# Performance work log

Measured on AMD Instinct MI355X. Metric: run time of the kernel, lower is better.

Reference implementation:

```python
import jax, jax.numpy as jnp
import numpy as np

H = 1024
B_SZ = 4
L = 2048


def setup_inputs() -> dict:
    key = jax.random.key(0)
    ks = jax.random.split(key, 7)
    s_in = 1.0 / np.sqrt(H)
    x = jax.random.normal(ks[0], (B_SZ, L, H), dtype=jnp.float32)
    # torch nn.Linear weights: (out_features, in_features)
    W_proj = jax.random.uniform(ks[1], (4 * H, H), minval=-s_in, maxval=s_in, dtype=jnp.float32)
    W_delta = jax.random.uniform(ks[2], (H, H), minval=-s_in, maxval=s_in, dtype=jnp.float32)
    b_delta = jax.random.uniform(ks[3], (H,), minval=-s_in, maxval=s_in, dtype=jnp.float32)
    A = 0.02 * jax.random.normal(ks[4], (1, 1, H), dtype=jnp.float32)
    Bp = 0.02 * jax.random.normal(ks[5], (1, H, 1), dtype=jnp.float32)
    D = jnp.ones((1,), dtype=jnp.float32)
    return {"x": x, "W_proj": W_proj, "A": A, "Bp": Bp, "D": D, "W_delta": W_delta, "b_delta": b_delta}


def reference(x, W_proj, A, Bp, D, W_delta, b_delta):
    # x: (b, l, h)
    h = x.shape[-1]
    proj = x @ W_proj.T                                   # (b, l, 4h)
    delta, Bs, Cs, residual = jnp.split(proj, 4, axis=-1) # each (b, l, h)
    delta = jax.nn.softplus(delta @ W_delta.T + b_delta)  # (b, l, h)
    A1 = A[0, 0]       # (h,)
    B1 = Bp[0, :, 0]   # (h,)
    # discretization: dA[b,h,l] = exp(delta*A)[b,l,h] * B1[h] (n-dim of Bp has size 1)
    dA = jnp.exp(delta * A1) * B1                         # (b, l, h), layout transposed vs torch
    # dB[b,h,0,l] = cumsum_l(delta[b,l,h] * B1[h])
    dB = jnp.cumsum(delta * B1, axis=1)                   # (b, l, h)
    # selective_scan: y[b,h,l] = sum_n (dA[b,h,l]*u[b,h,n] + dB[b,h,0,l]) * C[b,h,n]
    # sum over n distributes: y = dA * sum_n(u*C) + dB * sum_n(C)
    uC = jnp.sum(x * Cs, axis=1, keepdims=True)           # (b, 1, h)
    Csum = jnp.sum(Cs, axis=1, keepdims=True)             # (b, 1, h)
    y = dA * uC + dB * Csum                               # (b, l, h)
    return y + residual * D
```

## Files before the change

kernel.cpp:

```cpp
#include <hip/hip_runtime.h>
#include <hip/hip_bf16.h>
#include <cstdint>

#define H 1024
#define BSZ 4
#define LSEQ 2048
#define M_TOT (BSZ*LSEQ)
#define NCH 32
#define LCH (LSEQ/NCH)

typedef __attribute__((ext_vector_type(4))) float  f32x4;
typedef __attribute__((ext_vector_type(2))) float  f32x2;
typedef __attribute__((ext_vector_type(8))) __bf16 bf16x8;
typedef __attribute__((ext_vector_type(4))) __bf16 bf16x4;
typedef __attribute__((ext_vector_type(2))) __bf16 bf16x2;

typedef __attribute__((address_space(1))) unsigned int as1_u32;
typedef __attribute__((address_space(3))) unsigned int as3_u32;

__device__ __forceinline__ void gld_lds16(const void* g, const void* l) {
    as1_u32* gp = reinterpret_cast<as1_u32*>((uintptr_t)g);
    as3_u32* lp = reinterpret_cast<as3_u32*>((uint32_t)(uintptr_t)l);
    __builtin_amdgcn_global_load_lds(gp, lp, 16, 0, 0);
}

__device__ __forceinline__ float softplus_fast(float f) {
    return fmaxf(f, 0.f) + __logf(1.f + __expf(-fabsf(f)));
}

template<int KT, int MODE>
__global__ __launch_bounds__(256, 3) void gemm_bt(
    const __bf16* __restrict__ A,
    const __bf16* __restrict__ B,
    __bf16* __restrict__ O0,
    __bf16* __restrict__ O2,
    const __bf16* __restrict__ xb,
    const float* __restrict__ bias,
    float* __restrict__ pD,
    float* __restrict__ pUp,
    float* __restrict__ pCp)
{
    constexpr int K = KT * 32;
    __shared__ __align__(16) __bf16 lds[17408];

    const int tid  = threadIdx.x;
    const int lane = tid & 63;
    const int wid  = tid >> 6;
    const int wr   = (wid >> 1) * 64;
    const int wc   = (wid & 1) * 64;
    const int l15  = lane & 15;
    const int quad = lane >> 4;

    const int row0 = blockIdx.y * 128;
    const int col0 = blockIdx.x * 128;

    const int srow = lane >> 2;
    const int soct = (lane & 3) ^ ((lane >> 3) & 3);
    const __bf16* ag0 = A + (size_t)(row0 + (wid    )*16 + srow) * K + soct*8;
    const __bf16* ag1 = A + (size_t)(row0 + (wid + 4)*16 + srow) * K + soct*8;
    const __bf16* bg0 = B + (size_t)(col0 + (wid    )*16 + srow) * K + soct*8;
    const __bf16* bg1 = B + (size_t)(col0 + (wid + 4)*16 + srow) * K + soct*8;
    const int lA0 = (wid    )*512;
    const int lA1 = (wid + 4)*512;
    const int lB0 = 4096 + (wid    )*512;
    const int lB1 = 4096 + (wid + 4)*512;

    const int sw = (l15 >> 1) & 3;
    int aoff[4], boff[4];
#pragma unroll
    for (int i = 0; i < 4; ++i) {
        aoff[i] =        ((wr + i*16 + l15) * 4 + (quad ^ sw)) * 8;
        boff[i] = 4096 + ((wc + i*16 + l15) * 4 + (quad ^ sw)) * 8;
    }

    f32x4 acc[4][4] = {};

    auto stage = [&](int buf) {
        __bf16* base = lds + buf * 8192;
        gld_lds16(ag0, base + lA0);
        gld_lds16(ag1, base + lA1);
        gld_lds16(bg0, base + lB0);
        gld_lds16(bg1, base + lB1);
        ag0 += 32; ag1 += 32; bg0 += 32; bg1 += 32;
    };
    auto compute = [&](int buf) {
        const __bf16* base = lds + buf * 8192;
        bf16x8 af[4], bf[4];
#pragma unroll
        for (int i = 0; i < 4; ++i) af[i] = *(const bf16x8*)(base + aoff[i]);
#pragma unroll
        for (int j = 0; j < 4; ++j) bf[j] = *(const bf16x8*)(base + boff[j]);
#pragma unroll
        for (int i = 0; i < 4; ++i)
#pragma unroll
            for (int j = 0; j < 4; ++j)
                acc[i][j] = __builtin_amdgcn_mfma_f32_16x16x32_bf16(
                    af[i], bf[j], acc[i][j], 0, 0, 0);
    };

    stage(0);
#pragma unroll 2
    for (int kt = 0; kt < KT; ++kt) {
        __syncthreads();
        if (kt + 1 < KT) stage((kt + 1) & 1);
        compute(kt & 1);
    }

    const int colb = (col0 & 1023) + wc + l15;
    const int rowb = row0 + wr + quad*4;

    if (MODE == 0) {
#pragma unroll
        for (int i = 0; i < 4; ++i)
#pragma unroll
            for (int j = 0; j < 4; ++j) {
                const int col = colb + j*16;
#pragma unroll
                for (int r = 0; r < 4; ++r)
                    O0[(size_t)(rowb + i*16 + r) * H + col] = (__bf16)acc[i][j][r];
            }
    } else {
        const int seg = col0 >> 10;
        if (seg == 0) {
            const int chunk = (row0 + wr) >> 6;
#pragma unroll
            for (int j = 0; j < 4; ++j) {
                const int col = colb + j*16;
                const float bv = bias[col];
                float s = 0.f;
#pragma unroll
                for (int i = 0; i < 4; ++i)
#pragma unroll
                    for (int r = 0; r < 4; ++r) {
                        float f = softplus_fast(acc[i][j][r] + bv);
                        O0[(size_t)(rowb + i*16 + r) * H + col] = (__bf16)f;
                        s += f;
                    }
                s += __shfl_down(s, 32); s += __shfl_down(s, 16);
                if (quad == 0) pD[chunk*H + col] = s;
            }
        } else if (seg == 1) {
            __syncthreads();
#pragma unroll
            for (int i = 0; i < 4; ++i)
#pragma unroll
                for (int j = 0; j < 4; ++j) {
                    const int lrow0 = wr + quad*4 + i*16;
                    const int lcol  = wc + j*16 + l15;
#pragma unroll
                    for (int r = 0; r < 4; ++r)
                        lds[(lrow0 + r)*136 + lcol] = (__bf16)acc[i][j][r];
                }
            __syncthreads();
            const int g   = tid >> 4;
            const int oct = tid & 15;
            const int gc0 = (col0 & 1023) + oct*8;
            float su[8] = {}, sc[8] = {};
#pragma unroll
            for (int rr = 0; rr < 8; ++rr) {
                const int lrow = g*8 + rr;
                bf16x8 cv = *(const bf16x8*)(lds + lrow*136 + oct*8);
                bf16x8 xv = *(const bf16x8*)(xb + (size_t)(row0 + lrow)*H + gc0);
#pragma unroll
                for (int q = 0; q < 8; ++q) {
                    float c = (float)cv[q];
                    su[q] += (float)xv[q] * c;
                    sc[q] += c;
                }
            }
            float* pf = reinterpret_cast<float*>(lds);
            __syncthreads();
#pragma unroll
            for (int q = 0; q < 8; ++q) {
                pf[g*128 + oct*8 + q]        = su[q];
                pf[2048 + g*128 + oct*8 + q] = sc[q];
            }
            __syncthreads();
            const int col = tid & 127;
            const int rb  = row0 >> 7;
            float s = 0.f;
            if (tid < 128) {
#pragma unroll
                for (int g2 = 0; g2 < 16; ++g2) s += pf[g2*128 + col];
                pUp[rb*H + (col0 & 1023) + col] = s;
            } else {
#pragma unroll
                for (int g2 = 0; g2 < 16; ++g2) s += pf[2048 + g2*128 + col];
                pCp[rb*H + (col0 & 1023) + col] = s;
            }
        } else {
#pragma unroll
            for (int i = 0; i < 4; ++i)
#pragma unroll
                for (int j = 0; j < 4; ++j) {
                    const int col = colb + j*16;
#pragma unroll
                    for (int r = 0; r < 4; ++r)
                        O2[(size_t)(rowb + i*16 + r) * H + col] = (__bf16)acc[i][j][r];
                }
        }
    }
}

#define XB 8192
#define PB 2048
#define DB 1024
#define TB 256
__global__ void cast_kernel(const float* __restrict__ x,
                            const float* __restrict__ Wp,
                            const float* __restrict__ Wd,
                            __bf16* __restrict__ xb,
                            __bf16* __restrict__ Wpb,
                            __bf16* __restrict__ Wdb,
                            __bf16* __restrict__ Wp1T)
{
    __shared__ __bf16 tlds[64*65];
    const int t = threadIdx.x;
    const int bidx = blockIdx.x;

    if (bidx < XB + PB + DB) {
        const f32x4* src; __bf16* dst; int si, di;
        if (bidx < XB) {
            int i = bidx*256 + t;
            src = (const f32x4*)x;  si = i; dst = xb;  di = i;
        } else if (bidx < XB + PB) {
            int j = (bidx - XB)*256 + t;
            int row = j >> 8, cf = j & 255;
            src = (const f32x4*)Wp; si = (2048 + row)*256 + cf;
            dst = Wpb; di = (1024 + row)*256 + cf;
        } else {
            int j = (bidx - XB - PB)*256 + t;
            src = (const f32x4*)Wd; si = j; dst = Wdb; di = j;
        }
        f32x4 v = src[si];
        bf16x4 o = { (__bf16)v[0], (__bf16)v[1], (__bf16)v[2], (__bf16)v[3] };
        *(bf16x4*)(dst + (size_t)di*4) = o;
    } else {
        int tt = bidx - (XB + PB + DB);
        int ty = tt >> 4, tx = tt & 15;
        int rb = t >> 4, cb = t & 15;
#pragma unroll
        for (int rr = 0; rr < 4; ++rr) {
            int row = rb*4 + rr;
            f32x4 v = *(const f32x4*)(Wp + (size_t)(ty*64 + row)*1024 + tx*64 + cb*4);
#pragma unroll
            for (int q = 0; q < 4; ++q)
                tlds[row*65 + cb*4 + q] = (__bf16)v[q];
        }
        __syncthreads();
#pragma unroll
        for (int rr = 0; rr < 4; ++rr) {
            int kk = rb*4 + rr;
            bf16x4 o = { tlds[(cb*4+0)*65 + kk], tlds[(cb*4+1)*65 + kk],
                         tlds[(cb*4+2)*65 + kk], tlds[(cb*4+3)*65 + kk] };
            *(bf16x4*)(Wp1T + (size_t)(tx*64 + kk)*1024 + ty*64 + cb*4) = o;
        }
    }
}

__global__ void final_kernel(const __bf16* __restrict__ delta,
                             const __bf16* __restrict__ res,
                             const float* __restrict__ pD,
                             const float* __restrict__ pUp,
                             const float* __restrict__ pCp,
                             const float* __restrict__ Av,
                             const float* __restrict__ Bv,
                             const float* __restrict__ Dv,
                             float* __restrict__ out)
{
    const int c = blockIdx.x, b = blockIdx.z;
    const int h0 = blockIdx.y * 512 + threadIdx.x * 2;
    float run0 = 0.f, run1 = 0.f;
    for (int cp = 0; cp < c; ++cp) {
        f32x2 v = *(const f32x2*)(pD + (b*NCH + cp)*H + h0);
        run0 += v[0]; run1 += v[1];
    }
    float uc0 = 0.f, uc1 = 0.f, cs0 = 0.f, cs1 = 0.f;
#pragma unroll
    for (int i = 0; i < 16; ++i) {
        f32x2 u = *(const f32x2*)(pUp + (b*16 + i)*H + h0);
        f32x2 s = *(const f32x2*)(pCp + (b*16 + i)*H + h0);
        uc0 += u[0]; uc1 += u[1]; cs0 += s[0]; cs1 += s[1];
    }
    const f32x2 a1 = *(const f32x2*)(Av + h0);
    const f32x2 b1 = *(const f32x2*)(Bv + h0);
    const float dd = Dv[0];
    size_t base = ((size_t)(b*LSEQ + c*LCH)) * H + h0;
    for (int l = 0; l < LCH; ++l) {
        size_t idx = base + (size_t)l * H;
        bf16x2 dv2 = *(const bf16x2*)(delta + idx);
        bf16x2 rs2 = *(const bf16x2*)(res + idx);
        float d0 = (float)dv2[0], d1v = (float)dv2[1];
        run0 += d0; run1 += d1v;
        f32x2 o;
        o[0] = __expf(d0*a1[0])*b1[0]*uc0 + run0*b1[0]*cs0 + (float)rs2[0]*dd;
        o[1] = __expf(d1v*a1[1])*b1[1]*uc1 + run1*b1[1]*cs1 + (float)rs2[1]*dd;
        *(f32x2*)(out + idx) = o;
    }
}

extern "C" void kernel_launch(void* const* d_in, const int* in_sizes, int n_in,
                              void* d_out, int out_size, void* d_ws, size_t ws_size,
                              hipStream_t stream)
{
    (void)in_sizes; (void)n_in; (void)out_size; (void)ws_size;
    const float* x  = (const float*)d_in[0];
    const float* Wp = (const float*)d_in[1];
    const float* Av = (const float*)d_in[2];
    const float* Bv = (const float*)d_in[3];
    const float* Dv = (const float*)d_in[4];
    const float* Wd = (const float*)d_in[5];
    const float* bd = (const float*)d_in[6];
    float* out = (float*)d_out;

    char* ws = (char*)d_ws;
    size_t o = 0;
    auto alloc = [&](size_t bytes) {
        void* p = ws + o; o += (bytes + 255) & ~(size_t)255; return p;
    };
    __bf16* xb   = (__bf16*)alloc((size_t)M_TOT * H * 2);
    __bf16* Wpb  = (__bf16*)alloc((size_t)3072 * H * 2);
    __bf16* Wdb  = (__bf16*)alloc((size_t)H * H * 2);
    __bf16* Wp1T = (__bf16*)alloc((size_t)H * H * 2);
    __bf16* resb = (__bf16*)alloc((size_t)M_TOT * H * 2);
    __bf16* db   = (__bf16*)alloc((size_t)M_TOT * H * 2);
    float*  pD   = (float*)alloc((size_t)BSZ * NCH * H * 4);
    float*  pUp  = (float*)alloc((size_t)64 * H * 4);
    float*  pCp  = (float*)alloc((size_t)64 * H * 4);

    cast_kernel<<<XB + PB + DB + TB, 256, 0, stream>>>(
        x, Wp, Wd, xb, Wpb, Wdb, Wp1T);
    gemm_bt<32, 0><<<dim3(8, 8), 256, 0, stream>>>(
        Wdb, Wp1T, Wpb, nullptr, nullptr, nullptr, nullptr, nullptr, nullptr);
    gemm_bt<32, 2><<<dim3(24, 64), 256, 0, stream>>>(
        xb, Wpb, db, resb, xb, bd, pD, pUp, pCp);
    final_kernel<<<dim3(NCH, 2, BSZ), 256, 0, stream>>>(db, resb, pD, pUp, pCp,
                                                        Av, Bv, Dv, out);
}
```

Before: 206.0 us.

## Replace main projection GEMM with 256x256-tile, 8-wave software-pipelined kernel

The large x@W_proj GEMM moves from a 128x128-tile kernel with 4 waves to a new 256x256-tile kernel with 8 waves and 128 KB of double-buffered LDS. Loads go straight to LDS through an XOR swizzle and are interleaved with MFMA phases using explicit barriers, vmcnt waits and setprio. The fused epilogues (softplus with chunk sums, the uC/Csum reductions, the residual store) are rewritten for the larger tile, and a swizzled grid order is added for L2 locality. This is meant to increase data reuse and overlap memory with compute, but it raises register and LDS pressure, and only 384 blocks may leave the device underfilled.

```diff
diff --git a/kernel.cpp b/kernel.cpp
--- a/kernel.cpp
+++ b/kernel.cpp
@@ -119,85 +119,225 @@
                 for (int r = 0; r < 4; ++r)
                     O0[(size_t)(rowb + i*16 + r) * H + col] = (__bf16)acc[i][j][r];
             }
-    } else {
-        const int seg = col0 >> 10;
-        if (seg == 0) {
-            const int chunk = (row0 + wr) >> 6;
-#pragma unroll
-            for (int j = 0; j < 4; ++j) {
-                const int col = colb + j*16;
-                const float bv = bias[col];
+    }
+    (void)xb; (void)bias; (void)pD; (void)pUp; (void)pCp; (void)O2;
+}
+
+
+#define BAR()    asm volatile("s_barrier" ::: "memory")
+#define WAITV2() asm volatile("s_waitcnt vmcnt(2)" ::: "memory")
+
+#define STAGE_A(d, h, kt) do {                                               \
+    const __bf16* g_ = Asrc + (size_t)((h)*128) * H + (kt)*64;               \
+    const __bf16* l_ = lds + (d)*32768 + ((h)*128)*64 + lwave;               \
+    gld_lds16(g_,          l_);                                              \
+    gld_lds16(g_ + 64*H,   l_ + 64*64);                                      \
+} while(0)
+
+#define STAGE_B(d, h, kt) do {                                               \
+    const __bf16* g_ = Bsrc + (size_t)((h)*128) * H + (kt)*64;               \
+    const __bf16* l_ = lds + (d)*32768 + 16384 + ((h)*128)*64 + lwave;       \
+    gld_lds16(g_,          l_);                                              \
+    gld_lds16(g_ + 64*H,   l_ + 64*64);                                      \
+} while(0)
+
+#define RD_A(d, mh) do {                                                     \
+    const __bf16* base_ = lds + (d)*32768;                                   \
+    _Pragma("unroll")                                                        \
+    for (int ii = 0; ii < 4; ++ii) {                                         \
+        af[ii][0] = *(const bf16x8*)(base_ + aoff[(mh)*4 + ii]);             \
+        af[ii][1] = *(const bf16x8*)(base_ + (aoff[(mh)*4 + ii] ^ 32));      \
+    }                                                                        \
+} while(0)
+
+#define RD_B(d, nh) do {                                                     \
+    const __bf16* base_ = lds + (d)*32768;                                   \
+    _Pragma("unroll")                                                        \
+    for (int jj = 0; jj < 2; ++jj) {                                         \
+        bf[(nh)*2+jj][0] = *(const bf16x8*)(base_ + boff[(nh)*2 + jj]);      \
+        bf[(nh)*2+jj][1] = *(const bf16x8*)(base_ + (boff[(nh)*2 + jj] ^ 32)); \
+    }                                                                        \
+} while(0)
+
+#define MM(mh, nh) do {                                                      \
+    __builtin_amdgcn_s_setprio(1);                                           \
+    _Pragma("unroll")                                                        \
+    for (int ii = 0; ii < 4; ++ii)                                           \
+    _Pragma("unroll")                                                        \
+    for (int jj = 0; jj < 2; ++jj)                                           \
+    _Pragma("unroll")                                                        \
+    for (int kk = 0; kk < 2; ++kk)                                           \
+        acc[(mh)*4+ii][(nh)*2+jj] = __builtin_amdgcn_mfma_f32_16x16x32_bf16( \
+            af[ii][kk], bf[(nh)*2+jj][kk], acc[(mh)*4+ii][(nh)*2+jj], 0,0,0);\
+    __builtin_amdgcn_s_setprio(0);                                           \
+} while(0)
+
+__global__ __launch_bounds__(512, 2) void gemm256(
+    const __bf16* __restrict__ A,
+    const __bf16* __restrict__ B,
+    __bf16* __restrict__ O0,
+    __bf16* __restrict__ O2,
+    const __bf16* __restrict__ xb,
+    const float* __restrict__ bias,
+    float* __restrict__ pD,
+    float* __restrict__ pUp,
+    float* __restrict__ pCp)
+{
+    __shared__ __align__(16) __bf16 lds[65536];
+
+    const int tid  = threadIdx.x;
+    const int lane = tid & 63;
+    const int wid  = tid >> 6;
+    const int l15  = lane & 15;
+    const int quad = lane >> 4;
+    const int wrv  = (wid >> 2) * 128;
+    const int wcv  = (wid & 3) * 64;
+
+    const int bid = blockIdx.x;
+    const int swz = (bid & 7) * 48 + (bid >> 3);
+    const int bx = swz % 12;
+    const int by = swz / 12;
+    const int row0 = by * 256;
+    const int col0 = bx * 256;
+
+    const int lg = (tid & 7) ^ ((tid >> 3) & 7);
+    const __bf16* Asrc = A + (size_t)(row0 + (tid >> 3)) * H + lg * 8;
+    const __bf16* Bsrc = B + (size_t)(col0 + (tid >> 3)) * H + lg * 8;
+    const int lwave = wid * 8 * 64;
+
+    int aoff[8], boff[4];
+#pragma unroll
+    for (int i = 0; i < 8; ++i)
+        aoff[i] = (wrv + i*16 + l15)*64 + ((quad ^ (l15 & 7)) << 3);
+#pragma unroll
+    for (int j = 0; j < 4; ++j)
+        boff[j] = 16384 + (wcv + j*16 + l15)*64 + ((quad ^ (l15 & 7)) << 3);
+
+    f32x4 acc[8][4] = {};
+    bf16x8 af[4][2], bf[4][2];
+
+    STAGE_A(0,0,0); STAGE_A(0,1,0); STAGE_B(0,0,0); STAGE_B(0,1,0);
+    STAGE_A(1,0,1);
+
+#pragma unroll 1
+    for (int it = 0; it < 8; ++it) {
+        const int t1 = 2*it + 1;
+        const int t2 = (it < 7) ? 2*it + 2 : 15;
+        const int t3 = (it < 7) ? 2*it + 3 : 15;
+        WAITV2(); BAR();
+        RD_A(0,0); RD_B(0,0);
+        STAGE_A(1,1,t1);
+        BAR(); MM(0,0); BAR();
+        RD_B(0,1);
+        STAGE_B(1,0,t1);
+        BAR(); MM(0,1); BAR();
+        RD_A(0,1);
+        STAGE_B(1,1,t1);
+        BAR(); MM(1,0); BAR();
+        STAGE_A(0,0,t2);
+        BAR(); MM(1,1); BAR();
+        WAITV2(); BAR();
+        RD_A(1,0); RD_B(1,0);
+        STAGE_A(0,1,t2);
+        BAR(); MM(0,0); BAR();
+        RD_B(1,1);
+        STAGE_B(0,0,t2);
+        BAR(); MM(0,1); BAR();
+        RD_A(1,1);
+        STAGE_B(0,1,t2);
+        BAR(); MM(1,0); BAR();
+        STAGE_A(1,0,t3);
+        BAR(); MM(1,1); BAR();
+    }
+    asm volatile("s_waitcnt vmcnt(0)" ::: "memory");
+    __syncthreads();
+
+    const int seg   = col0 >> 10;
+    const int cbase = col0 & 1023;
+    const int colb  = cbase + wcv + l15;
+    const int rowb  = row0 + wrv + quad*4;
+
+    if (seg == 0) {
+        const int chunkb = (row0 + wrv) >> 6;
+#pragma unroll
+        for (int j = 0; j < 4; ++j) {
+            const int col = colb + j*16;
+            const float bv = bias[col];
+#pragma unroll
+            for (int ih = 0; ih < 2; ++ih) {
                 float s = 0.f;
 #pragma unroll
-                for (int i = 0; i < 4; ++i)
+                for (int ii = 0; ii < 4; ++ii) {
+                    const int i = ih*4 + ii;
 #pragma unroll
                     for (int r = 0; r < 4; ++r) {
                         float f = softplus_fast(acc[i][j][r] + bv);
                         O0[(size_t)(rowb + i*16 + r) * H + col] = (__bf16)f;
                         s += f;
                     }
+                }
                 s += __shfl_down(s, 32); s += __shfl_down(s, 16);
-                if (quad == 0) pD[chunk*H + col] = s;
+                if (quad == 0) pD[(chunkb + ih)*H + col] = s;
             }
-        } else if (seg == 1) {
-            __syncthreads();
-#pragma unroll
-            for (int i = 0; i < 4; ++i)
-#pragma unroll
-                for (int j = 0; j < 4; ++j) {
-                    const int lrow0 = wr + quad*4 + i*16;
-                    const int lcol  = wc + j*16 + l15;
-#pragma unroll
-                    for (int r = 0; r < 4; ++r)
-                        lds[(lrow0 + r)*136 + lcol] = (__bf16)acc[i][j][r];
-                }
-            __syncthreads();
-            const int g   = tid >> 4;
-            const int oct = tid & 15;
-            const int gc0 = (col0 & 1023) + oct*8;
-            float su[8] = {}, sc[8] = {};
-#pragma unroll
-            for (int rr = 0; rr < 8; ++rr) {
-                const int lrow = g*8 + rr;
-                bf16x8 cv = *(const bf16x8*)(lds + lrow*136 + oct*8);
-                bf16x8 xv = *(const bf16x8*)(xb + (size_t)(row0 + lrow)*H + gc0);
-#pragma unroll
-                for (int q = 0; q < 8; ++q) {
-                    float c = (float)cv[q];
-                    su[q] += (float)xv[q] * c;
-                    sc[q] += c;
+        }
+    } else if (seg == 2) {
+#pragma unroll
+        for (int i = 0; i < 8; ++i)
+#pragma unroll
+            for (int j = 0; j < 4; ++j) {
+                const int col = colb + j*16;
+#pragma unroll
+                for (int r = 0; r < 4; ++r)
+                    O2[(size_t)(rowb + i*16 + r) * H + col] = (__bf16)acc[i][j][r];
+            }
+    } else {
+#pragma unroll
+        for (int i = 0; i < 8; ++i)
+#pragma unroll
+            for (int j = 0; j < 4; ++j) {
+                const int lcol = wcv + j*16 + l15;
+#pragma unroll
+                for (int r = 0; r < 4; ++r) {
+                    const int lrow = wrv + i*16 + quad*4 + r;
+                    lds[lrow*256 + (((lcol>>3) ^ ((lrow>>2)&7))<<3) + (lcol&7)]
+                        = (__bf16)acc[i][j][r];
                 }
             }
-            float* pf = reinterpret_cast<float*>(lds);
-            __syncthreads();
+        __syncthreads();
+        const int g = tid >> 5, oct = tid & 31;
+        const int gc0 = cbase + oct*8;
+        float su[8] = {}, sc[8] = {};
+#pragma unroll
+        for (int rr = 0; rr < 16; ++rr) {
+            const int lrow = g*16 + rr;
+            bf16x8 cv = *(const bf16x8*)(lds + lrow*256 +
+                                         ((oct ^ ((lrow>>2)&7)) << 3));
+            bf16x8 xv = *(const bf16x8*)(xb + (size_t)(row0 + lrow)*H + gc0);
 #pragma unroll
             for (int q = 0; q < 8; ++q) {
-                pf[g*128 + oct*8 + q]        = su[q];
-                pf[2048 + g*128 + oct*8 + q] = sc[q];
+                float c = (float)cv[q];
+                su[q] += (float)xv[q] * c;
+                sc[q] += c;
             }
-            __syncthreads();
-            const int col = tid & 127;
-            const int rb  = row0 >> 7;
+        }
+        float* pf = reinterpret_cast<float*>(lds);
+        __syncthreads();
+#pragma unroll
+        for (int q = 0; q < 8; ++q) {
+            pf[g*256 + oct*8 + q]        = su[q];
+            pf[4096 + g*256 + oct*8 + q] = sc[q];
+        }
+        __syncthreads();
+        const int col = tid & 255;
+        const int sel = tid >> 8;
+#pragma unroll
+        for (int rb2 = 0; rb2 < 2; ++rb2) {
             float s = 0.f;
-            if (tid < 128) {
-#pragma unroll
-                for (int g2 = 0; g2 < 16; ++g2) s += pf[g2*128 + col];
-                pUp[rb*H + (col0 & 1023) + col] = s;
-            } else {
-#pragma unroll
-                for (int g2 = 0; g2 < 16; ++g2) s += pf[2048 + g2*128 + col];
-                pCp[rb*H + (col0 & 1023) + col] = s;
-            }
-        } else {
-#pragma unroll
-            for (int i = 0; i < 4; ++i)
-#pragma unroll
-                for (int j = 0; j < 4; ++j) {
-                    const int col = colb + j*16;
-#pragma unroll
-                    for (int r = 0; r < 4; ++r)
-                        O2[(size_t)(rowb + i*16 + r) * H + col] = (__bf16)acc[i][j][r];
-                }
+#pragma unroll
+            for (int g2 = 0; g2 < 8; ++g2)
+                s += pf[sel*4096 + (rb2*8 + g2)*256 + col];
+            float* dst = sel ? pCp : pUp;
+            dst[(size_t)((row0 >> 7) + rb2)*H + cbase + col] = s;
         }
     }
 }
@@ -332,7 +472,7 @@
         x, Wp, Wd, xb, Wpb, Wdb, Wp1T);
     gemm_bt<32, 0><<<dim3(8, 8), 256, 0, stream>>>(
         Wdb, Wp1T, Wpb, nullptr, nullptr, nullptr, nullptr, nullptr, nullptr);
-    gemm_bt<32, 2><<<dim3(24, 64), 256, 0, stream>>>(
+    gemm256<<<dim3(384), 512, 0, stream>>>(
         xb, Wpb, db, resb, xb, bd, pD, pUp, pCp);
     final_kernel<<<dim3(NCH, 2, BSZ), 256, 0, stream>>>(db, resb, pD, pUp, pCp,
                                                         Av, Bv, Dv, out);
```

Result: no change. 202.4 us (-1.8%).

## Replace main projection GEMM with 256x128 triple-buffered pipelined kernel

Applied to the files above, without the earlier changes.

Adds a new 512-thread GEMM kernel with 256x128 tiles, K-step 64, triple-buffered direct global-to-LDS loads with explicit vmcnt waits, split half-K fragment loads, s_setprio around MFMAs, and a grouped block swizzle for L2 reuse. It replaces the 128x128 double-buffered kernel for the main x @ W projection, aiming to hide load latency and raise MFMA utilisation. The C-segment reduction is rewritten to use an XOR-swizzled LDS layout without padding. The final kernel is relaunched with smaller blocks and more of them. The larger LDS footprint (144KB) limits occupancy, and the hand-written waits have to match the order in which stages are issued.

```diff
diff --git a/kernel.cpp b/kernel.cpp
--- a/kernel.cpp
+++ b/kernel.cpp
@@ -32,16 +32,10 @@
 __global__ __launch_bounds__(256, 3) void gemm_bt(
     const __bf16* __restrict__ A,
     const __bf16* __restrict__ B,
-    __bf16* __restrict__ O0,
-    __bf16* __restrict__ O2,
-    const __bf16* __restrict__ xb,
-    const float* __restrict__ bias,
-    float* __restrict__ pD,
-    float* __restrict__ pUp,
-    float* __restrict__ pCp)
+    __bf16* __restrict__ O0)
 {
     constexpr int K = KT * 32;
-    __shared__ __align__(16) __bf16 lds[17408];
+    __shared__ __align__(16) __bf16 lds[16384];
 
     const int tid  = threadIdx.x;
     const int lane = tid & 63;
@@ -106,10 +100,153 @@
         compute(kt & 1);
     }
 
-    const int colb = (col0 & 1023) + wc + l15;
+    const int colb = col0 + wc + l15;
     const int rowb = row0 + wr + quad*4;
-
-    if (MODE == 0) {
+#pragma unroll
+    for (int i = 0; i < 4; ++i)
+#pragma unroll
+        for (int j = 0; j < 4; ++j) {
+            const int col = colb + j*16;
+#pragma unroll
+            for (int r = 0; r < 4; ++r)
+                O0[(size_t)(rowb + i*16 + r) * H + col] = (__bf16)acc[i][j][r];
+        }
+}
+
+
+#define BAR()    asm volatile("s_barrier" ::: "memory")
+#define WAIT6()  asm volatile("s_waitcnt vmcnt(6)" ::: "memory")
+#define WAIT0()  asm volatile("s_waitcnt vmcnt(0)" ::: "memory")
+
+#define STA(b,u,kt) gld_lds16(Asrc + (size_t)((u)*64)*H + (kt)*64, \
+                              lds + (b)*24576 + (u)*4096 + lwb)
+#define STB(b,u,kt) gld_lds16(Bsrc + (size_t)((u)*64)*H + (kt)*64, \
+                              lds + (b)*24576 + 16384 + (u)*4096 + lwb)
+#define STAGE6(b,kt) do { STA(b,0,kt); STA(b,1,kt); STA(b,2,kt); STA(b,3,kt); \
+                          STB(b,0,kt); STB(b,1,kt); } while(0)
+
+#define TILE(bc,bn,kn,DS,WAITMAC) do {                                        \
+    WAITMAC();                                                                \
+    BAR();                                                                    \
+    { const __bf16* base_ = lds + (bc)*24576;                                 \
+      _Pragma("unroll")                                                       \
+      for (int i_ = 0; i_ < 4; ++i_)                                          \
+          af0[i_] = *(const bf16x8*)(base_ + aoff[i_]);                       \
+      _Pragma("unroll")                                                       \
+      for (int j_ = 0; j_ < 4; ++j_)                                          \
+          bf0[j_] = *(const bf16x8*)(base_ + boff[j_]); }                     \
+    if (DS) STAGE6(bn, kn);                                                   \
+    BAR();                                                                    \
+    __builtin_amdgcn_s_setprio(1);                                            \
+    _Pragma("unroll")                                                         \
+    for (int i_ = 0; i_ < 4; ++i_)                                            \
+    _Pragma("unroll")                                                         \
+    for (int j_ = 0; j_ < 4; ++j_)                                            \
+        acc[i_][j_] = __builtin_amdgcn_mfma_f32_16x16x32_bf16(                \
+            af0[i_], bf0[j_], acc[i_][j_], 0, 0, 0);                          \
+    __builtin_amdgcn_s_setprio(0);                                            \
+    BAR();                                                                    \
+    { const __bf16* base_ = lds + (bc)*24576;                                 \
+      _Pragma("unroll")                                                       \
+      for (int i_ = 0; i_ < 4; ++i_)                                          \
+          af1[i_] = *(const bf16x8*)(base_ + (aoff[i_] ^ 32));                \
+      _Pragma("unroll")                                                       \
+      for (int j_ = 0; j_ < 4; ++j_)                                          \
+          bf1[j_] = *(const bf16x8*)(base_ + (boff[j_] ^ 32)); }              \
+    BAR();                                                                    \
+    __builtin_amdgcn_s_setprio(1);                                            \
+    _Pragma("unroll")                                                         \
+    for (int i_ = 0; i_ < 4; ++i_)                                            \
+    _Pragma("unroll")                                                         \
+    for (int j_ = 0; j_ < 4; ++j_)                                            \
+        acc[i_][j_] = __builtin_amdgcn_mfma_f32_16x16x32_bf16(                \
+            af1[i_], bf1[j_], acc[i_][j_], 0, 0, 0);                          \
+    __builtin_amdgcn_s_setprio(0);                                            \
+} while(0)
+
+__global__ __launch_bounds__(512, 2) void gemm256b(
+    const __bf16* __restrict__ A,
+    const __bf16* __restrict__ B,
+    __bf16* __restrict__ O0,
+    __bf16* __restrict__ O2,
+    const __bf16* __restrict__ xb,
+    const float* __restrict__ bias,
+    float* __restrict__ pD,
+    float* __restrict__ pUp,
+    float* __restrict__ pCp)
+{
+    __shared__ __align__(16) __bf16 lds[73728];
+
+    const int tid  = threadIdx.x;
+    const int lane = tid & 63;
+    const int wid  = tid >> 6;
+    const int l15  = lane & 15;
+    const int quad = lane >> 4;
+    const int wrv  = (wid >> 1) * 64;
+    const int wcv  = (wid & 1) * 64;
+
+    const int bid = blockIdx.x;
+    const int swz = (bid & 7) * 96 + (bid >> 3);
+    const int bx = swz % 24;
+    const int by = swz / 24;
+    const int row0 = by * 256;
+    const int col0 = bx * 128;
+
+    const int lg = (tid & 7) ^ ((tid >> 3) & 7);
+    const __bf16* Asrc = A + (size_t)(row0 + (tid >> 3)) * H + lg * 8;
+    const __bf16* Bsrc = B + (size_t)(col0 + (tid >> 3)) * H + lg * 8;
+    const int lwb = wid * 512;
+
+    int aoff[4], boff[4];
+#pragma unroll
+    for (int i = 0; i < 4; ++i)
+        aoff[i] = (wrv + i*16 + l15)*64 + ((quad ^ (l15 & 7)) << 3);
+#pragma unroll
+    for (int j = 0; j < 4; ++j)
+        boff[j] = 16384 + (wcv + j*16 + l15)*64 + ((quad ^ (l15 & 7)) << 3);
+
+    f32x4 acc[4][4] = {};
+    bf16x8 af0[4], bf0[4], af1[4], bf1[4];
+
+    STAGE6(0, 0);
+    STAGE6(1, 1);
+
+#pragma unroll 1
+    for (int g = 0; g < 4; ++g) {
+        TILE(0, 2, 3*g + 2, 1, WAIT6);
+        TILE(1, 0, 3*g + 3, 1, WAIT6);
+        TILE(2, 1, 3*g + 4, 1, WAIT6);
+    }
+    TILE(0, 2, 14, 1, WAIT6);
+    TILE(1, 0, 15, 1, WAIT6);
+    TILE(2, 0,  0, 0, WAIT6);
+    TILE(0, 0,  0, 0, WAIT0);
+    __syncthreads();
+
+    const int seg   = col0 >> 10;
+    const int cbase = col0 & 1023;
+    const int colb  = cbase + wcv + l15;
+    const int rowb  = row0 + wrv + quad*4;
+
+    if (seg == 0) {
+        const int chunk = (row0 + wrv) >> 6;
+#pragma unroll
+        for (int j = 0; j < 4; ++j) {
+            const int col = colb + j*16;
+            const float bv = bias[col];
+            float s = 0.f;
+#pragma unroll
+            for (int i = 0; i < 4; ++i)
+#pragma unroll
+                for (int r = 0; r < 4; ++r) {
+                    float f = softplus_fast(acc[i][j][r] + bv);
+                    O0[(size_t)(rowb + i*16 + r) * H + col] = (__bf16)f;
+                    s += f;
+                }
+            s += __shfl_down(s, 32); s += __shfl_down(s, 16);
+            if (quad == 0) pD[chunk*H + col] = s;
+        }
+    } else if (seg == 2) {
 #pragma unroll
         for (int i = 0; i < 4; ++i)
 #pragma unroll
@@ -117,88 +254,55 @@
                 const int col = colb + j*16;
 #pragma unroll
                 for (int r = 0; r < 4; ++r)
-                    O0[(size_t)(rowb + i*16 + r) * H + col] = (__bf16)acc[i][j][r];
+                    O2[(size_t)(rowb + i*16 + r) * H + col] = (__bf16)acc[i][j][r];
             }
     } else {
-        const int seg = col0 >> 10;
-        if (seg == 0) {
-            const int chunk = (row0 + wr) >> 6;
+#pragma unroll
+        for (int i = 0; i < 4; ++i)
 #pragma unroll
             for (int j = 0; j < 4; ++j) {
-                const int col = colb + j*16;
-                const float bv = bias[col];
-                float s = 0.f;
-#pragma unroll
-                for (int i = 0; i < 4; ++i)
-#pragma unroll
-                    for (int r = 0; r < 4; ++r) {
-                        float f = softplus_fast(acc[i][j][r] + bv);
-                        O0[(size_t)(rowb + i*16 + r) * H + col] = (__bf16)f;
-                        s += f;
-                    }
-                s += __shfl_down(s, 32); s += __shfl_down(s, 16);
-                if (quad == 0) pD[chunk*H + col] = s;
-            }
-        } else if (seg == 1) {
-            __syncthreads();
-#pragma unroll
-            for (int i = 0; i < 4; ++i)
-#pragma unroll
-                for (int j = 0; j < 4; ++j) {
-                    const int lrow0 = wr + quad*4 + i*16;
-                    const int lcol  = wc + j*16 + l15;
-#pragma unroll
-                    for (int r = 0; r < 4; ++r)
-                        lds[(lrow0 + r)*136 + lcol] = (__bf16)acc[i][j][r];
-                }
-            __syncthreads();
-            const int g   = tid >> 4;
-            const int oct = tid & 15;
-            const int gc0 = (col0 & 1023) + oct*8;
-            float su[8] = {}, sc[8] = {};
-#pragma unroll
-            for (int rr = 0; rr < 8; ++rr) {
-                const int lrow = g*8 + rr;
-                bf16x8 cv = *(const bf16x8*)(lds + lrow*136 + oct*8);
-                bf16x8 xv = *(const bf16x8*)(xb + (size_t)(row0 + lrow)*H + gc0);
-#pragma unroll
-                for (int q = 0; q < 8; ++q) {
-                    float c = (float)cv[q];
-                    su[q] += (float)xv[q] * c;
-                    sc[q] += c;
+                const int lcol = wcv + j*16 + l15;
+#pragma unroll
+                for (int r = 0; r < 4; ++r) {
+                    const int lrow = wrv + i*16 + quad*4 + r;
+                    lds[lrow*128 + (((lcol>>3) ^ (lrow&15)) << 3) + (lcol&7)]
+                        = (__bf16)acc[i][j][r];
                 }
             }
-            float* pf = reinterpret_cast<float*>(lds);
-            __syncthreads();
+        __syncthreads();
+        const int g = tid >> 4, oct = tid & 15;
+        const int gc0 = cbase + oct*8;
+        float su[8] = {}, sc[8] = {};
+#pragma unroll
+        for (int rr = 0; rr < 8; ++rr) {
+            const int lrow = g*8 + rr;
+            bf16x8 cv = *(const bf16x8*)(lds + lrow*128 +
+                                         ((oct ^ (lrow&15)) << 3));
+            bf16x8 xv = *(const bf16x8*)(xb + (size_t)(row0 + lrow)*H + gc0);
 #pragma unroll
             for (int q = 0; q < 8; ++q) {
-                pf[g*128 + oct*8 + q]        = su[q];
-                pf[2048 + g*128 + oct*8 + q] = sc[q];
+                float c = (float)cv[q];
+                su[q] += (float)xv[q] * c;
+                sc[q] += c;
             }
-            __syncthreads();
-            const int col = tid & 127;
-            const int rb  = row0 >> 7;
-            float s = 0.f;
-            if (tid < 128) {
-#pragma unroll
-                for (int g2 = 0; g2 < 16; ++g2) s += pf[g2*128 + col];
-                pUp[rb*H + (col0 & 1023) + col] = s;
-            } else {
-#pragma unroll
-                for (int g2 = 0; g2 < 16; ++g2) s += pf[2048 + g2*128 + col];
-                pCp[rb*H + (col0 & 1023) + col] = s;
-            }
-        } else {
-#pragma unroll
-            for (int i = 0; i < 4; ++i)
-#pragma unroll
-                for (int j = 0; j < 4; ++j) {
-                    const int col = colb + j*16;
-#pragma unroll
-                    for (int r = 0; r < 4; ++r)
-                        O2[(size_t)(rowb + i*16 + r) * H + col] = (__bf16)acc[i][j][r];
-                }
-        }
+        }
+        float* pf = reinterpret_cast<float*>(lds);
+        __syncthreads();
+#pragma unroll
+        for (int q = 0; q < 8; ++q) {
+            pf[g*128 + oct*8 + q]        = su[q];
+            pf[4096 + g*128 + oct*8 + q] = sc[q];
+        }
+        __syncthreads();
+        const int col = tid & 127;
+        const int rb  = (tid >> 7) & 1;
+        const int arr = tid >> 8;
+        float s = 0.f;
+#pragma unroll
+        for (int g2 = 0; g2 < 16; ++g2)
+            s += pf[arr*4096 + (rb*16 + g2)*128 + col];
+        float* dst = arr ? pCp : pUp;
+        dst[(size_t)((row0 >> 7) + rb)*H + cbase + col] = s;
     }
 }
 
@@ -269,7 +373,7 @@
                              float* __restrict__ out)
 {
     const int c = blockIdx.x, b = blockIdx.z;
-    const int h0 = blockIdx.y * 512 + threadIdx.x * 2;
+    const int h0 = blockIdx.y * 256 + threadIdx.x * 2;
     float run0 = 0.f, run1 = 0.f;
     for (int cp = 0; cp < c; ++cp) {
         f32x2 v = *(const f32x2*)(pD + (b*NCH + cp)*H + h0);
@@ -330,10 +434,9 @@
 
     cast_kernel<<<XB + PB + DB + TB, 256, 0, stream>>>(
         x, Wp, Wd, xb, Wpb, Wdb, Wp1T);
-    gemm_bt<32, 0><<<dim3(8, 8), 256, 0, stream>>>(
-        Wdb, Wp1T, Wpb, nullptr, nullptr, nullptr, nullptr, nullptr, nullptr);
-    gemm_bt<32, 2><<<dim3(24, 64), 256, 0, stream>>>(
+    gemm_bt<32, 0><<<dim3(8, 8), 256, 0, stream>>>(Wdb, Wp1T, Wpb);
+    gemm256b<<<dim3(768), 512, 0, stream>>>(
         xb, Wpb, db, resb, xb, bd, pD, pUp, pCp);
-    final_kernel<<<dim3(NCH, 2, BSZ), 256, 0, stream>>>(db, resb, pD, pUp, pCp,
+    final_kernel<<<dim3(NCH, 4, BSZ), 128, 0, stream>>>(db, resb, pD, pUp, pCp,
                                                         Av, Bv, Dv, out);
 }
```

Result: faster. 200.3 us (-2.8%).

## Replace main projection GEMM with hybrid 256x256/256x128 tile kernel with explicit pipelining

Applied to the files above, without the earlier changes.

The main x@W GEMM moves to a new 512-thread kernel. It uses 256x256 tiles for the delta and C segments and 256x128 tiles for the residual segment, with double-buffered direct-to-LDS loads, XOR-swizzled LDS, manual barriers, s_setprio around MFMA blocks, and a tile-order remap. The aim is more data reuse per tile and better overlap of global loads with MFMA, while keeping the softplus and C-reduction epilogues fused. The final kernel's launch is reshaped to smaller blocks. The cost is 128KB of LDS per block, which limits occupancy, plus more complex synchronisation.

```diff
diff --git a/kernel.cpp b/kernel.cpp
--- a/kernel.cpp
+++ b/kernel.cpp
@@ -28,20 +28,17 @@
     return fmaxf(f, 0.f) + __logf(1.f + __expf(-fabsf(f)));
 }
 
-template<int KT, int MODE>
+#define BAR()    asm volatile("s_barrier" ::: "memory")
+#define WAIT0()  asm volatile("s_waitcnt vmcnt(0)" ::: "memory")
+
+template<int KT>
 __global__ __launch_bounds__(256, 3) void gemm_bt(
     const __bf16* __restrict__ A,
     const __bf16* __restrict__ B,
-    __bf16* __restrict__ O0,
-    __bf16* __restrict__ O2,
-    const __bf16* __restrict__ xb,
-    const float* __restrict__ bias,
-    float* __restrict__ pD,
-    float* __restrict__ pUp,
-    float* __restrict__ pCp)
+    __bf16* __restrict__ O0)
 {
     constexpr int K = KT * 32;
-    __shared__ __align__(16) __bf16 lds[17408];
+    __shared__ __align__(16) __bf16 lds[16384];
 
     const int tid  = threadIdx.x;
     const int lane = tid & 63;
@@ -106,60 +103,169 @@
         compute(kt & 1);
     }
 
-    const int colb = (col0 & 1023) + wc + l15;
+    const int colb = col0 + wc + l15;
     const int rowb = row0 + wr + quad*4;
-
-    if (MODE == 0) {
-#pragma unroll
-        for (int i = 0; i < 4; ++i)
-#pragma unroll
-            for (int j = 0; j < 4; ++j) {
-                const int col = colb + j*16;
-#pragma unroll
-                for (int r = 0; r < 4; ++r)
-                    O0[(size_t)(rowb + i*16 + r) * H + col] = (__bf16)acc[i][j][r];
-            }
-    } else {
-        const int seg = col0 >> 10;
+#pragma unroll
+    for (int i = 0; i < 4; ++i)
+#pragma unroll
+        for (int j = 0; j < 4; ++j) {
+            const int col = colb + j*16;
+#pragma unroll
+            for (int r = 0; r < 4; ++r)
+                O0[(size_t)(rowb + i*16 + r) * H + col] = (__bf16)acc[i][j][r];
+        }
+}
+
+
+__global__ __launch_bounds__(512, 2) void gemm_hyb(
+    const __bf16* __restrict__ A,
+    const __bf16* __restrict__ B,
+    __bf16* __restrict__ O0,
+    __bf16* __restrict__ O2,
+    const __bf16* __restrict__ xb,
+    const float* __restrict__ bias,
+    float* __restrict__ pD,
+    float* __restrict__ pUp,
+    float* __restrict__ pCp)
+{
+    __shared__ __align__(16) __bf16 lds[65536];
+
+    const int tid  = threadIdx.x;
+    const int lane = tid & 63;
+    const int wid  = tid >> 6;
+    const int l15  = lane & 15;
+    const int quad = lane >> 4;
+    const int bid  = blockIdx.x;
+
+    const int lg  = (tid & 7) ^ ((tid >> 3) & 7);
+    const int lwb = wid * 512;
+
+    if (bid < 256) {
+        const int s  = (bid & 7) * 32 + (bid >> 3);
+        const int bx = s >> 5;
+        const int by = s & 31;
+        const int row0 = by * 256;
+        const int col0 = bx * 256;
+
+        const __bf16* Asrc = A + (size_t)(row0 + (tid >> 3)) * H + lg * 8;
+        const __bf16* Bsrc = B + (size_t)(col0 + (tid >> 3)) * H + lg * 8;
+
+        const int wrv = (wid >> 2) * 128;
+        const int wcv = (wid & 3) * 64;
+
+        int aoff[8], boff[4];
+#pragma unroll
+        for (int i = 0; i < 8; ++i)
+            aoff[i] = (wrv + i*16 + l15)*64 + ((quad ^ (l15 & 7)) << 3);
+#pragma unroll
+        for (int j = 0; j < 4; ++j)
+            boff[j] = 16384 + (wcv + j*16 + l15)*64 + ((quad ^ (l15 & 7)) << 3);
+
+        f32x4 acc[8][4] = {};
+        bf16x8 af0[4], af1[4], bf[4];
+
+        auto stageA = [&](int buf, int kt) {
+#pragma unroll
+            for (int u = 0; u < 4; ++u)
+                gld_lds16(Asrc + (size_t)(u*64)*H + kt*64,
+                          lds + buf*32768 + u*4096 + lwb);
+        };
+        auto stageB = [&](int buf, int kt) {
+#pragma unroll
+            for (int u = 0; u < 4; ++u)
+                gld_lds16(Bsrc + (size_t)(u*64)*H + kt*64,
+                          lds + buf*32768 + 16384 + u*4096 + lwb);
+        };
+        auto rdA = [&](bf16x8 (&dst)[4], const __bf16* base, int half, int x) {
+#pragma unroll
+            for (int i = 0; i < 4; ++i)
+                dst[i] = *(const bf16x8*)(base + (aoff[half*4 + i] ^ x));
+        };
+        auto rdB = [&](const __bf16* base, int x) {
+#pragma unroll
+            for (int j = 0; j < 4; ++j)
+                bf[j] = *(const bf16x8*)(base + (boff[j] ^ x));
+        };
+        auto mm = [&](bf16x8 (&af)[4], int mh) {
+            __builtin_amdgcn_s_setprio(1);
+#pragma unroll
+            for (int i = 0; i < 4; ++i)
+#pragma unroll
+                for (int j = 0; j < 4; ++j)
+                    acc[mh*4 + i][j] = __builtin_amdgcn_mfma_f32_16x16x32_bf16(
+                        af[i], bf[j], acc[mh*4 + i][j], 0, 0, 0);
+            __builtin_amdgcn_s_setprio(0);
+        };
+
+        stageA(0, 0); stageB(0, 0);
+#pragma unroll 1
+        for (int t = 0; t < 16; ++t) {
+            const int cb = t & 1, nb = cb ^ 1;
+            const __bf16* base = lds + cb*32768;
+            WAIT0(); BAR();
+            rdA(af0, base, 0, 0); rdB(base, 0);
+            if (t < 15) stageA(nb, t + 1);
+            BAR(); mm(af0, 0); BAR();
+            rdA(af1, base, 1, 0);
+            if (t < 15) stageB(nb, t + 1);
+            BAR(); mm(af1, 1); BAR();
+            rdA(af0, base, 0, 32); rdB(base, 32);
+            BAR(); mm(af0, 0); BAR();
+            rdA(af1, base, 1, 32);
+            BAR(); mm(af1, 1); BAR();
+        }
+
+        const int seg   = col0 >> 10;
+        const int cbase = col0 & 1023;
+        const int colb  = cbase + wcv + l15;
+        const int rowb  = row0 + wrv + quad*4;
+
         if (seg == 0) {
-            const int chunk = (row0 + wr) >> 6;
+            const int chunkb = (row0 + wrv) >> 6;
 #pragma unroll
             for (int j = 0; j < 4; ++j) {
                 const int col = colb + j*16;
                 const float bv = bias[col];
-                float s = 0.f;
-#pragma unroll
-                for (int i = 0; i < 4; ++i)
+#pragma unroll
+                for (int ih = 0; ih < 2; ++ih) {
+                    float sacc = 0.f;
+#pragma unroll
+                    for (int ii = 0; ii < 4; ++ii) {
+                        const int i = ih*4 + ii;
+#pragma unroll
+                        for (int r = 0; r < 4; ++r) {
+                            float f = softplus_fast(acc[i][j][r] + bv);
+                            O0[(size_t)(rowb + i*16 + r) * H + col] = (__bf16)f;
+                            sacc += f;
+                        }
+                    }
+                    sacc += __shfl_down(sacc, 32); sacc += __shfl_down(sacc, 16);
+                    if (quad == 0) pD[(chunkb + ih)*H + col] = sacc;
+                }
+            }
+        } else {
+            __syncthreads();
+#pragma unroll
+            for (int i = 0; i < 8; ++i)
+#pragma unroll
+                for (int j = 0; j < 4; ++j) {
+                    const int lcol = wcv + j*16 + l15;
 #pragma unroll
                     for (int r = 0; r < 4; ++r) {
-                        float f = softplus_fast(acc[i][j][r] + bv);
-                        O0[(size_t)(rowb + i*16 + r) * H + col] = (__bf16)f;
-                        s += f;
+                        const int lrow = wrv + i*16 + quad*4 + r;
+                        lds[lrow*256 + (((lcol>>3) ^ ((lrow>>2)&7))<<3) + (lcol&7)]
+                            = (__bf16)acc[i][j][r];
                     }
-                s += __shfl_down(s, 32); s += __shfl_down(s, 16);
-                if (quad == 0) pD[chunk*H + col] = s;
-            }
-        } else if (seg == 1) {
-            __syncthreads();
-#pragma unroll
-            for (int i = 0; i < 4; ++i)
-#pragma unroll
-                for (int j = 0; j < 4; ++j) {
-                    const int lrow0 = wr + quad*4 + i*16;
-                    const int lcol  = wc + j*16 + l15;
-#pragma unroll
-                    for (int r = 0; r < 4; ++r)
-                        lds[(lrow0 + r)*136 + lcol] = (__bf16)acc[i][j][r];
                 }
             __syncthreads();
-            const int g   = tid >> 4;
-            const int oct = tid & 15;
-            const int gc0 = (col0 & 1023) + oct*8;
+            const int g = tid >> 5, oct = tid & 31;
+            const int gc0 = cbase + oct*8;
             float su[8] = {}, sc[8] = {};
 #pragma unroll
-            for (int rr = 0; rr < 8; ++rr) {
-                const int lrow = g*8 + rr;
-                bf16x8 cv = *(const bf16x8*)(lds + lrow*136 + oct*8);
+            for (int rr = 0; rr < 16; ++rr) {
+                const int lrow = g*16 + rr;
+                bf16x8 cv = *(const bf16x8*)(lds + lrow*256 +
+                                             ((oct ^ ((lrow>>2)&7)) << 3));
                 bf16x8 xv = *(const bf16x8*)(xb + (size_t)(row0 + lrow)*H + gc0);
 #pragma unroll
                 for (int q = 0; q < 8; ++q) {
@@ -172,33 +278,103 @@
             __syncthreads();
 #pragma unroll
             for (int q = 0; q < 8; ++q) {
-                pf[g*128 + oct*8 + q]        = su[q];
-                pf[2048 + g*128 + oct*8 + q] = sc[q];
+                pf[g*256 + oct*8 + q]        = su[q];
+                pf[4096 + g*256 + oct*8 + q] = sc[q];
             }
             __syncthreads();
-            const int col = tid & 127;
-            const int rb  = row0 >> 7;
-            float s = 0.f;
-            if (tid < 128) {
-#pragma unroll
-                for (int g2 = 0; g2 < 16; ++g2) s += pf[g2*128 + col];
-                pUp[rb*H + (col0 & 1023) + col] = s;
-            } else {
-#pragma unroll
-                for (int g2 = 0; g2 < 16; ++g2) s += pf[2048 + g2*128 + col];
-                pCp[rb*H + (col0 & 1023) + col] = s;
+            const int col = tid & 255;
+            const int sel = tid >> 8;
+#pragma unroll
+            for (int rb2 = 0; rb2 < 2; ++rb2) {
+                float sv = 0.f;
+#pragma unroll
+                for (int g2 = 0; g2 < 8; ++g2)
+                    sv += pf[sel*4096 + (rb2*8 + g2)*256 + col];
+                float* dst = sel ? pCp : pUp;
+                dst[(size_t)((row0 >> 7) + rb2)*H + cbase + col] = sv;
             }
-        } else {
+        }
+    } else {
+        const int sb = bid - 256;
+        const int s  = (sb & 7) * 32 + (sb >> 3);
+        const int bx = s >> 5;
+        const int by = s & 31;
+        const int row0 = by * 256;
+        const int col0 = 2048 + bx * 128;
+
+        const __bf16* Asrc = A + (size_t)(row0 + (tid >> 3)) * H + lg * 8;
+        const __bf16* Bsrc = B + (size_t)(col0 + (tid >> 3)) * H + lg * 8;
+
+        const int wrv = (wid >> 1) * 64;
+        const int wcv = (wid & 1) * 64;
+
+        int aoff[4], boff[4];
+#pragma unroll
+        for (int i = 0; i < 4; ++i)
+            aoff[i] = (wrv + i*16 + l15)*64 + ((quad ^ (l15 & 7)) << 3);
+#pragma unroll
+        for (int j = 0; j < 4; ++j)
+            boff[j] = 16384 + (wcv + j*16 + l15)*64 + ((quad ^ (l15 & 7)) << 3);
+
+        f32x4 acc[4][4] = {};
+        bf16x8 af[4], bf[4];
+
+        auto stageA = [&](int buf, int kt) {
+#pragma unroll
+            for (int u = 0; u < 4; ++u)
+                gld_lds16(Asrc + (size_t)(u*64)*H + kt*64,
+                          lds + buf*32768 + u*4096 + lwb);
+        };
+        auto stageB = [&](int buf, int kt) {
+#pragma unroll
+            for (int u = 0; u < 2; ++u)
+                gld_lds16(Bsrc + (size_t)(u*64)*H + kt*64,
+                          lds + buf*32768 + 16384 + u*4096 + lwb);
+        };
+        auto rdAB = [&](const __bf16* base, int x) {
 #pragma unroll
             for (int i = 0; i < 4; ++i)
-#pragma unroll
-                for (int j = 0; j < 4; ++j) {
-                    const int col = colb + j*16;
-#pragma unroll
-                    for (int r = 0; r < 4; ++r)
-                        O2[(size_t)(rowb + i*16 + r) * H + col] = (__bf16)acc[i][j][r];
-                }
-        }
+                af[i] = *(const bf16x8*)(base + (aoff[i] ^ x));
+#pragma unroll
+            for (int j = 0; j < 4; ++j)
+                bf[j] = *(const bf16x8*)(base + (boff[j] ^ x));
+        };
+        auto mm = [&]() {
+            __builtin_amdgcn_s_setprio(1);
+#pragma unroll
+            for (int i = 0; i < 4; ++i)
+#pragma unroll
+                for (int j = 0; j < 4; ++j)
+                    acc[i][j] = __builtin_amdgcn_mfma_f32_16x16x32_bf16(
+                        af[i], bf[j], acc[i][j], 0, 0, 0);
+            __builtin_amdgcn_s_setprio(0);
+        };
+
+        stageA(0, 0); stageB(0, 0);
+#pragma unroll 1
+        for (int t = 0; t < 16; ++t) {
+            const int cb = t & 1, nb = cb ^ 1;
+            const __bf16* base = lds + cb*32768;
+            WAIT0(); BAR();
+            rdAB(base, 0);
+            if (t < 15) stageA(nb, t + 1);
+            BAR(); mm(); BAR();
+            rdAB(base, 32);
+            if (t < 15) stageB(nb, t + 1);
+            BAR(); mm(); BAR();
+        }
+
+        const int colb = bx*128 + wcv + l15;
+        const int rowb = row0 + wrv + quad*4;
+#pragma unroll
+        for (int i = 0; i < 4; ++i)
+#pragma unroll
+            for (int j = 0; j < 4; ++j) {
+                const int col = colb + j*16;
+#pragma unroll
+                for (int r = 0; r < 4; ++r)
+                    O2[(size_t)(rowb + i*16 + r) * H + col] = (__bf16)acc[i][j][r];
+            }
     }
 }
 
@@ -269,7 +445,7 @@
                              float* __restrict__ out)
 {
     const int c = blockIdx.x, b = blockIdx.z;
-    const int h0 = blockIdx.y * 512 + threadIdx.x * 2;
+    const int h0 = blockIdx.y * 256 + threadIdx.x * 2;
     float run0 = 0.f, run1 = 0.f;
     for (int cp = 0; cp < c; ++cp) {
         f32x2 v = *(const f32x2*)(pD + (b*NCH + cp)*H + h0);
@@ -330,10 +506,9 @@
 
     cast_kernel<<<XB + PB + DB + TB, 256, 0, stream>>>(
         x, Wp, Wd, xb, Wpb, Wdb, Wp1T);
-    gemm_bt<32, 0><<<dim3(8, 8), 256, 0, stream>>>(
-        Wdb, Wp1T, Wpb, nullptr, nullptr, nullptr, nullptr, nullptr, nullptr);
-    gemm_bt<32, 2><<<dim3(24, 64), 256, 0, stream>>>(
+    gemm_bt<32><<<dim3(8, 8), 256, 0, stream>>>(Wdb, Wp1T, Wpb);
+    gemm_hyb<<<dim3(512), 512, 0, stream>>>(
         xb, Wpb, db, resb, xb, bd, pD, pUp, pCp);
-    final_kernel<<<dim3(NCH, 2, BSZ), 256, 0, stream>>>(db, resb, pD, pUp, pCp,
+    final_kernel<<<dim3(NCH, 4, BSZ), 128, 0, stream>>>(db, resb, pD, pUp, pCp,
                                                         Av, Bv, Dv, out);
 }
```

Result: slower. 223.5 us (+8.5%).
